# Kernel optimization log

Hardware: AMD Instinct MI355X
Metric: run time of the kernel (lower is better)

The kernel has to match this reference:

```python
import jax, jax.numpy as jnp
import numpy as np

VJ = 80      # vjointnum (groups)
FS = 480     # feature_size = 2*k of RFF
HD = 256     # hidden_dim
K = 240      # RFF k
BATCH = 2048
TWO_PI = 2.0 * np.pi
SLOPE = 0.01  # LeakyReLU default negative_slope


def _wn(v, g):
    # weight_norm (dim=0): w[o,:] = g[o] * v[o,:] / ||v[o,:]||
    return v * (g[:, None] / jnp.linalg.norm(v, axis=1, keepdims=True))


def _grouped(x, v, g, b):
    # x: [B, G, in_g]; v: [G*out_g, in_g]; equivalent to groups=G Conv1d with kernel 1
    w = _wn(v, g)
    out_g = w.shape[0] // VJ
    y = jnp.einsum('bgi,goi->bgo', x, w.reshape(VJ, out_g, -1))
    return y + b.reshape(VJ, out_g)


def _lrelu(t):
    return jnp.where(t >= 0, t, SLOPE * t)


def setup_inputs() -> dict:
    key = jax.random.key(0)
    ks = jax.random.split(key, 12)
    d = {
        'querypoint': jax.random.normal(ks[0], (BATCH, VJ, 3), jnp.float32),
        'point_features': jax.random.normal(ks[1], (BATCH, VJ, FS), jnp.float32),
        'B_rff': jax.random.normal(ks[2], (3, K), jnp.float32),  # std=1
    }
    # per-group layer sizes: 480->512, 512->512, 512->256, 256->6
    dims = [(FS, 2 * HD), (2 * HD, 2 * HD), (2 * HD, HD), (HD, 6)]
    for i, (din, dout) in enumerate(dims):
        d[f'v{i}'] = jax.random.normal(ks[3 + 2 * i], (VJ * dout, din), jnp.float32) * 0.02
        d[f'g{i}'] = jnp.ones((VJ * dout,), jnp.float32)
        d[f'b{i}'] = jnp.zeros((VJ * dout,), jnp.float32)
    return d


def reference(querypoint, point_features, B_rff,
              v0, g0, b0, v1, g1, b1, v2, g2, b2, v3, g3, b3):
    # RFF encode: [B, N, 480]
    emb = TWO_PI * jnp.einsum('bnd,dk->bnk', querypoint, B_rff)
    feat = jnp.concatenate([jnp.cos(emb), jnp.sin(emb)], axis=-1)
    x = point_features + feat                       # [B, 80, 480]
    Bsz = x.shape[0]
    # transpose(-2,-1) then reshape(B, C*N, 1) with groups=80 ==> [B, 80, 480]
    x = jnp.transpose(x, (0, 2, 1)).reshape(Bsz, VJ, FS)
    x = _lrelu(_grouped(x, v0, g0, b0))             # [B, 80, 512]
    x = _lrelu(_grouped(x, v1, g1, b1))             # [B, 80, 512]
    x = _lrelu(_grouped(x, v2, g2, b2))             # [B, 80, 256]
    y = _grouped(x, v3, g3, b3)                     # [B, 80, 6]
    return y.reshape(Bsz, VJ, 6)
```

## Files before the change

### kernel.cpp

```cpp
#include <hip/hip_runtime.h>


typedef __attribute__((ext_vector_type(8))) short short8;
typedef __attribute__((ext_vector_type(4))) float f32x4;
typedef __attribute__((ext_vector_type(4))) unsigned short ushort4v;
typedef __attribute__((ext_vector_type(2))) unsigned int uint2v;

#define VJ    80
#define FS    480
#define HD2   512
#define HD    256
#define BATCH 2048
#define SMLP  528

static __device__ __forceinline__ unsigned short f2bf(float f) {
  unsigned int u = __builtin_bit_cast(unsigned int, f);
  u += 0x7FFFu + ((u >> 16) & 1u);
  return (unsigned short)(u >> 16);
}
static __device__ __forceinline__ float bf2f(unsigned short h) {
  unsigned int u = ((unsigned int)h) << 16;
  return __builtin_bit_cast(float, u);
}

template<int K, int RPG>
static __device__ __forceinline__ void wfrag_body(
    int blk, const float* __restrict__ v, const float* __restrict__ gain,
    unsigned short* __restrict__ dst, float* sV, float* sScale) {
  constexpr int KK = K / 32;
  constexpr int KP = K + 4;
  const int t  = threadIdx.x;
  const int n0 = blk * 16;
  const int g  = n0 / RPG;
  const int ni = (n0 % RPG) >> 4;

  const f32x4* v4 = (const f32x4*)(v + (size_t)n0 * K);
  for (int idx = t; idx < 16 * K / 4; idx += 256) {
    int row = idx / (K / 4), rem = idx - row * (K / 4);
    *(f32x4*)&sV[row * KP + rem * 4] = v4[idx];
  }
  __syncthreads();

  const int wave = t >> 6, lane = t & 63;
  for (int r = wave; r < 16; r += 4) {
    float s = 0.f;
    for (int k = lane; k < K; k += 64) { float x = sV[r * KP + k]; s += x * x; }
    #pragma unroll
    for (int off = 32; off > 0; off >>= 1) s += __shfl_down(s, off);
    if (lane == 0) sScale[r] = gain[n0 + r] / sqrtf(s);
  }
  __syncthreads();

  unsigned short* db = dst + (size_t)g * RPG * K + (size_t)ni * KK * 512;
  for (int o = t; o < 2 * K; o += 256) {
    int f  = o >> 6, l = o & 63;
    int nl = l & 15, k0 = (f << 5) + (((l >> 4) & 3) << 3);
    float sc = sScale[nl];
    short8 pk;
    #pragma unroll
    for (int j = 0; j < 8; ++j) pk[j] = (short)f2bf(sV[nl * KP + k0 + j] * sc);
    *(short8*)&db[(size_t)f * 512 + l * 8] = pk;
  }
}

static __device__ __forceinline__ void wrow_body(
    int blk, const float* __restrict__ v, const float* __restrict__ gain,
    unsigned short* __restrict__ wout, int rows, int din) {
  int row  = blk * 4 + (threadIdx.x >> 6);
  int lane = threadIdx.x & 63;
  if (row >= rows) return;
  const float* vr = v + (size_t)row * din;
  float s = 0.f;
  for (int k = lane; k < din; k += 64) { float x = vr[k]; s += x * x; }
  #pragma unroll
  for (int off = 32; off > 0; off >>= 1) s += __shfl_down(s, off);
  s = __shfl(s, 0);
  float scale = gain[row] / sqrtf(s);
  unsigned short* wr = wout + (size_t)row * din;
  for (int k = lane; k < din; k += 64) wr[k] = f2bf(vr[k] * scale);
}

__global__ void __launch_bounds__(256)
prep_weights(const float* __restrict__ v0, const float* __restrict__ g0,
             const float* __restrict__ v1, const float* __restrict__ g1,
             const float* __restrict__ v2, const float* __restrict__ g2,
             const float* __restrict__ v3, const float* __restrict__ g3,
             unsigned short* __restrict__ W0, unsigned short* __restrict__ W1,
             unsigned short* __restrict__ W2, unsigned short* __restrict__ W3) {
  __shared__ float sV[16 * 516];
  __shared__ float sScale[16];
  const int b = blockIdx.x;
  if      (b < 2560) wfrag_body<480, 512>(b,        v0, g0, W0, sV, sScale);
  else if (b < 5120) wfrag_body<512, 512>(b - 2560, v1, g1, W1, sV, sScale);
  else if (b < 6400) wfrag_body<512, 256>(b - 5120, v2, g2, W2, sV, sScale);
  else               wrow_body(b - 6400, v3, g3, W3, VJ * 6, HD);
}

__global__ void __launch_bounds__(1024)
prep_x(const float* __restrict__ qp, const float* __restrict__ pf,
       const float* __restrict__ Brff, unsigned short* __restrict__ Xg) {
  __shared__ float sB[720];
  __shared__ float sQ[240];
  __shared__ unsigned short sX[480 * 82];
  const int b = blockIdx.x;
  const int t = threadIdx.x;
  if (t < 720) sB[t] = Brff[t];
  if (t < 240) sQ[t] = qp[(size_t)b * 240 + t];
  __syncthreads();
  const float* pfb = pf + (size_t)b * 38400;
  #pragma unroll 2
  for (int idx = t; idx < 19200; idx += 1024) {
    int n2 = idx / 480;
    int c  = idx - n2 * 480;
    int n  = n2 * 2;
    int k  = (c < 240) ? c : c - 240;
    float bx = sB[k], by = sB[240 + k], bz = sB[480 + k];
    float d0 = sQ[n*3]   * bx + sQ[n*3+1] * by + sQ[n*3+2] * bz;
    float d1 = sQ[n*3+3] * bx + sQ[n*3+4] * by + sQ[n*3+5] * bz;
    float f0 = (c < 240) ? __builtin_amdgcn_cosf(d0) : __builtin_amdgcn_sinf(d0);
    float f1 = (c < 240) ? __builtin_amdgcn_cosf(d1) : __builtin_amdgcn_sinf(d1);
    unsigned int w = (unsigned int)f2bf(pfb[n * 480 + c] + f0)
                   | ((unsigned int)f2bf(pfb[(n + 1) * 480 + c] + f1) << 16);
    *(unsigned int*)&sX[c * 82 + n] = w;
  }
  __syncthreads();
  for (int idx4 = t; idx4 < 9600; idx4 += 1024) {
    int g  = idx4 / 120;
    int i4 = idx4 - g * 120;
    int i  = i4 * 4;
    int cl = i / 80;
    int n  = i - cl * 80;
    const unsigned int* p = (const unsigned int*)&sX[(g * 6 + cl) * 82 + n];
    uint2v val = { p[0], p[1] };
    *(uint2v*)(Xg + ((size_t)g * BATCH + b) * 480 + i) = val;
  }
}

#define MLP_STEP(kkv, B)                                                      \
  {                                                                           \
    const int kkc = (kkv);                                                    \
    __builtin_amdgcn_s_setprio(1);                                            \
    _Pragma("unroll")                                                         \
    for (int mi = 0; mi < 4; ++mi) {                                          \
      short8 a = *(const short8*)(aB + mi * 16 * SMLP + kkc * 32);            \
      _Pragma("unroll")                                                       \
      for (int ni = 0; ni < NF; ++ni)                                         \
        acc[mi][ni] = __builtin_amdgcn_mfma_f32_16x16x32_bf16(a, B[ni], acc[mi][ni], 0, 0, 0); \
    }                                                                         \
    __builtin_amdgcn_s_setprio(0);                                            \
    if (kkc + 2 < KK) {                                                       \
      _Pragma("unroll")                                                       \
      for (int ni = 0; ni < NF; ++ni)                                         \
        B[ni] = *(const short8*)(wB + ((size_t)ni * KK + kkc + 2) * 512);     \
    }                                                                         \
  }

template<int K, int N, bool ACT>
static __device__ __forceinline__ void run_layer8(
    unsigned short* __restrict__ s,
    const unsigned short* __restrict__ Wf, const float* __restrict__ bias,
    int wn, int lane) {
  constexpr int NF = N / 128;
  constexpr int KK = K / 32;
  const int nbase = wn * (N / 8);
  const int lr = lane & 15, lh = lane >> 4;

  f32x4 acc[4][NF];
  #pragma unroll
  for (int mi = 0; mi < 4; ++mi)
    #pragma unroll
    for (int ni = 0; ni < NF; ++ni) acc[mi][ni] = (f32x4){0.f, 0.f, 0.f, 0.f};

  const unsigned short* aB = s + lr * SMLP + lh * 8;
  const unsigned short* wB = Wf + (size_t)(wn * NF) * KK * 512 + lane * 8;

  short8 bb0[NF], bb1[NF];
  #pragma unroll
  for (int ni = 0; ni < NF; ++ni) bb0[ni] = *(const short8*)(wB + ((size_t)ni * KK    ) * 512);
  #pragma unroll
  for (int ni = 0; ni < NF; ++ni) bb1[ni] = *(const short8*)(wB + ((size_t)ni * KK + 1) * 512);

  #pragma unroll
  for (int kk2 = 0; kk2 < KK / 2; ++kk2) {
    MLP_STEP(2 * kk2,     bb0);
    MLP_STEP(2 * kk2 + 1, bb1);
  }
  if (KK & 1) MLP_STEP(KK - 1, bb0);

  float bv[NF];
  #pragma unroll
  for (int ni = 0; ni < NF; ++ni) bv[ni] = bias[nbase + ni * 16 + lr];

  __syncthreads();
  #pragma unroll
  for (int mi = 0; mi < 4; ++mi)
    #pragma unroll
    for (int ni = 0; ni < NF; ++ni)
      #pragma unroll
      for (int r = 0; r < 4; ++r) {
        float val = acc[mi][ni][r] + bv[ni];
        if (ACT) val = (val >= 0.f) ? val : 0.01f * val;
        s[(mi * 16 + lh * 4 + r) * SMLP + (nbase + ni * 16 + lr)] = f2bf(val);
      }
  __syncthreads();
}

__global__ void __launch_bounds__(512, 4)
mlp_kernel(const unsigned short* __restrict__ Xg,
           const unsigned short* __restrict__ W0, const unsigned short* __restrict__ W1,
           const unsigned short* __restrict__ W2, const unsigned short* __restrict__ W3,
           const float* __restrict__ b0, const float* __restrict__ b1,
           const float* __restrict__ b2, const float* __restrict__ b3,
           float* __restrict__ out) {
  __shared__ unsigned short s[64 * SMLP];

  const int bid   = blockIdx.x;
  const int xcd   = bid & 7;
  const int local = bid >> 3;
  const int g     = xcd * 10 + (local >> 5);
  const int tile  = local & 31;
  const int m0    = tile * 64;

  const int tid  = threadIdx.x, lane = tid & 63;
  const int wn   = tid >> 6;

  const unsigned short* Xs = Xg + ((size_t)g * BATCH + m0) * 480;
  for (int idx = tid; idx < 64 * 60; idx += 512) {
    int row = idx / 60, c = idx - row * 60;
    *(short8*)&s[row * SMLP + c * 8] = *(const short8*)(Xs + (size_t)row * 480 + c * 8);
  }
  __syncthreads();

  run_layer8<480, 512, true>(s, W0 + (size_t)g * 512 * 480, b0 + g * 512, wn, lane);
  run_layer8<512, 512, true>(s, W1 + (size_t)g * 512 * 512, b1 + g * 512, wn, lane);
  run_layer8<512, 256, true>(s, W2 + (size_t)g * 256 * 512, b2 + g * 256, wn, lane);

  {
    const int m = tid >> 3, o = tid & 7;
    if (o < 6) {
      const unsigned short* hrow = s + m * SMLP;
      const unsigned short* w = W3 + ((size_t)g * 6 + o) * 256;
      float sum = 0.f;
      #pragma unroll 8
      for (int k4 = 0; k4 < 64; ++k4) {
        ushort4v hv = *(const ushort4v*)(hrow + k4 * 4);
        ushort4v wv = *(const ushort4v*)(w + k4 * 4);
        sum += bf2f(hv[0]) * bf2f(wv[0]) + bf2f(hv[1]) * bf2f(wv[1])
             + bf2f(hv[2]) * bf2f(wv[2]) + bf2f(hv[3]) * bf2f(wv[3]);
      }
      out[((size_t)(m0 + m) * VJ + g) * 6 + o] = sum + b3[g * 6 + o];
    }
  }
}

extern "C" void kernel_launch(void* const* d_in, const int* in_sizes, int n_in,
                              void* d_out, int out_size, void* d_ws, size_t ws_size,
                              hipStream_t stream) {
  const float* qp   = (const float*)d_in[0];
  const float* pf   = (const float*)d_in[1];
  const float* Brff = (const float*)d_in[2];
  const float* v0 = (const float*)d_in[3];  const float* g0 = (const float*)d_in[4];  const float* b0 = (const float*)d_in[5];
  const float* v1 = (const float*)d_in[6];  const float* g1 = (const float*)d_in[7];  const float* b1 = (const float*)d_in[8];
  const float* v2 = (const float*)d_in[9];  const float* g2 = (const float*)d_in[10]; const float* b2 = (const float*)d_in[11];
  const float* v3 = (const float*)d_in[12]; const float* g3 = (const float*)d_in[13]; const float* b3 = (const float*)d_in[14];

  unsigned short* W0 = (unsigned short*)d_ws;
  unsigned short* W1 = W0 + (size_t)VJ * HD2 * FS;
  unsigned short* W2 = W1 + (size_t)VJ * HD2 * HD2;
  unsigned short* W3 = W2 + (size_t)VJ * HD  * HD2;
  unsigned short* Xg = W3 + (size_t)VJ * 6 * HD;

  prep_weights<<<dim3(6520), dim3(256), 0, stream>>>(v0, g0, v1, g1, v2, g2, v3, g3,
                                                     W0, W1, W2, W3);
  prep_x<<<dim3(BATCH), dim3(1024), 0, stream>>>(qp, pf, Brff, Xg);
  mlp_kernel<<<dim3(VJ * 32), dim3(512), 0, stream>>>(Xg, W0, W1, W2, W3,
                                                      b0, b1, b2, b3, (float*)d_out);
}
```

Measured before the change: 447.2 us.

## Switch MLP layers to 32x32x16 MFMA tiles and use MFMA for final layer

Rewrites the grouped MLP layers to use 32x32x16 bf16 MFMA instructions with 2 M-tiles per wave, replacing 16x16x32 with 4 M-tiles. The weight prep kernel now emits fragments matching the 32-wide layout with 512-thread blocks. The last 256->6 layer moves from a scalar dot product to a padded 16x16x32 MFMA using a new fragment-packed W3. The aim is fewer LDS A-fragment reads per MFMA and a cheaper final layer, in exchange for larger accumulator register use and more complex output indexing.

```diff
diff --git a/kernel.cpp b/kernel.cpp
--- a/kernel.cpp
+++ b/kernel.cpp
@@ -1,10 +1,11 @@
 #include <hip/hip_runtime.h>
 
 
-typedef __attribute__((ext_vector_type(8))) short short8;
-typedef __attribute__((ext_vector_type(4))) float f32x4;
-typedef __attribute__((ext_vector_type(4))) unsigned short ushort4v;
-typedef __attribute__((ext_vector_type(2))) unsigned int uint2v;
+typedef __attribute__((ext_vector_type(8)))  short short8;
+typedef __attribute__((ext_vector_type(4)))  float f32x4;
+typedef __attribute__((ext_vector_type(16))) float f32x16;
+typedef __attribute__((ext_vector_type(4)))  unsigned short ushort4v;
+typedef __attribute__((ext_vector_type(2)))  unsigned int uint2v;
 
 #define VJ    80
 #define FS    480
@@ -18,31 +19,27 @@
   u += 0x7FFFu + ((u >> 16) & 1u);
   return (unsigned short)(u >> 16);
 }
-static __device__ __forceinline__ float bf2f(unsigned short h) {
-  unsigned int u = ((unsigned int)h) << 16;
-  return __builtin_bit_cast(float, u);
-}
 
 template<int K, int RPG>
-static __device__ __forceinline__ void wfrag_body(
+static __device__ __forceinline__ void wfrag32_body(
     int blk, const float* __restrict__ v, const float* __restrict__ gain,
     unsigned short* __restrict__ dst, float* sV, float* sScale) {
-  constexpr int KK = K / 32;
+  constexpr int KS = K / 16;
   constexpr int KP = K + 4;
   const int t  = threadIdx.x;
-  const int n0 = blk * 16;
+  const int n0 = blk * 32;
   const int g  = n0 / RPG;
-  const int ni = (n0 % RPG) >> 4;
+  const int nt = (n0 % RPG) >> 5;
 
   const f32x4* v4 = (const f32x4*)(v + (size_t)n0 * K);
-  for (int idx = t; idx < 16 * K / 4; idx += 256) {
+  for (int idx = t; idx < 32 * K / 4; idx += 512) {
     int row = idx / (K / 4), rem = idx - row * (K / 4);
     *(f32x4*)&sV[row * KP + rem * 4] = v4[idx];
   }
   __syncthreads();
 
   const int wave = t >> 6, lane = t & 63;
-  for (int r = wave; r < 16; r += 4) {
+  for (int r = wave; r < 32; r += 8) {
     float s = 0.f;
     for (int k = lane; k < K; k += 64) { float x = sV[r * KP + k]; s += x * x; }
     #pragma unroll
@@ -51,49 +48,63 @@
   }
   __syncthreads();
 
-  unsigned short* db = dst + (size_t)g * RPG * K + (size_t)ni * KK * 512;
-  for (int o = t; o < 2 * K; o += 256) {
-    int f  = o >> 6, l = o & 63;
-    int nl = l & 15, k0 = (f << 5) + (((l >> 4) & 3) << 3);
+  unsigned short* db = dst + (size_t)g * RPG * K + (size_t)nt * KS * 512;
+  for (int o = t; o < KS * 64; o += 512) {
+    int ks = o >> 6, l = o & 63;
+    int nl = l & 31, k0 = ks * 16 + ((l >> 5) << 3);
     float sc = sScale[nl];
     short8 pk;
     #pragma unroll
     for (int j = 0; j < 8; ++j) pk[j] = (short)f2bf(sV[nl * KP + k0 + j] * sc);
-    *(short8*)&db[(size_t)f * 512 + l * 8] = pk;
-  }
-}
-
-static __device__ __forceinline__ void wrow_body(
-    int blk, const float* __restrict__ v, const float* __restrict__ gain,
-    unsigned short* __restrict__ wout, int rows, int din) {
-  int row  = blk * 4 + (threadIdx.x >> 6);
-  int lane = threadIdx.x & 63;
-  if (row >= rows) return;
-  const float* vr = v + (size_t)row * din;
-  float s = 0.f;
-  for (int k = lane; k < din; k += 64) { float x = vr[k]; s += x * x; }
-  #pragma unroll
-  for (int off = 32; off > 0; off >>= 1) s += __shfl_down(s, off);
-  s = __shfl(s, 0);
-  float scale = gain[row] / sqrtf(s);
-  unsigned short* wr = wout + (size_t)row * din;
-  for (int k = lane; k < din; k += 64) wr[k] = f2bf(vr[k] * scale);
-}
-
-__global__ void __launch_bounds__(256)
+    *(short8*)&db[(size_t)ks * 512 + l * 8] = pk;
+  }
+}
+
+static __device__ __forceinline__ void w3frag_body(
+    int gidx, const float* __restrict__ v3, const float* __restrict__ g3,
+    unsigned short* __restrict__ W3f, float* sV, float* sScale) {
+  const int t = threadIdx.x;
+  const f32x4* v4 = (const f32x4*)(v3 + (size_t)gidx * 6 * 256);
+  if (t < 384) {
+    int row = t >> 6, rem = t & 63;
+    *(f32x4*)&sV[row * 260 + rem * 4] = v4[t];
+  }
+  __syncthreads();
+  const int wave = t >> 6, lane = t & 63;
+  if (wave < 6) {
+    float s = 0.f;
+    #pragma unroll
+    for (int k = 0; k < 4; ++k) { float x = sV[wave * 260 + lane + k * 64]; s += x * x; }
+    #pragma unroll
+    for (int off = 32; off > 0; off >>= 1) s += __shfl_down(s, off);
+    if (lane == 0) sScale[wave] = g3[gidx * 6 + wave] / sqrtf(s);
+  }
+  __syncthreads();
+  {
+    int ks = t >> 6, l = t & 63;
+    int c = l & 15, k0 = ks * 32 + ((l >> 4) << 3);
+    short8 pk;
+    #pragma unroll
+    for (int j = 0; j < 8; ++j)
+      pk[j] = (c < 6) ? (short)f2bf(sV[c * 260 + k0 + j] * sScale[c]) : (short)0;
+    *(short8*)&W3f[(size_t)gidx * 4096 + (size_t)ks * 512 + l * 8] = pk;
+  }
+}
+
+__global__ void __launch_bounds__(512)
 prep_weights(const float* __restrict__ v0, const float* __restrict__ g0,
              const float* __restrict__ v1, const float* __restrict__ g1,
              const float* __restrict__ v2, const float* __restrict__ g2,
              const float* __restrict__ v3, const float* __restrict__ g3,
              unsigned short* __restrict__ W0, unsigned short* __restrict__ W1,
-             unsigned short* __restrict__ W2, unsigned short* __restrict__ W3) {
-  __shared__ float sV[16 * 516];
-  __shared__ float sScale[16];
+             unsigned short* __restrict__ W2, unsigned short* __restrict__ W3f) {
+  __shared__ float sV[32 * 516];
+  __shared__ float sScale[32];
   const int b = blockIdx.x;
-  if      (b < 2560) wfrag_body<480, 512>(b,        v0, g0, W0, sV, sScale);
-  else if (b < 5120) wfrag_body<512, 512>(b - 2560, v1, g1, W1, sV, sScale);
-  else if (b < 6400) wfrag_body<512, 256>(b - 5120, v2, g2, W2, sV, sScale);
-  else               wrow_body(b - 6400, v3, g3, W3, VJ * 6, HD);
+  if      (b < 1280) wfrag32_body<480, 512>(b,        v0, g0, W0, sV, sScale);
+  else if (b < 2560) wfrag32_body<512, 512>(b - 1280, v1, g1, W1, sV, sScale);
+  else if (b < 3200) wfrag32_body<512, 256>(b - 2560, v2, g2, W2, sV, sScale);
+  else               w3frag_body(b - 3200, v3, g3, W3f, sV, sScale);
 }
 
 __global__ void __launch_bounds__(1024)
@@ -136,71 +147,74 @@
   }
 }
 
-#define MLP_STEP(kkv, B)                                                      \
+#define MLP_STEP32(ksv, BB)                                                   \
   {                                                                           \
-    const int kkc = (kkv);                                                    \
+    const int ksc = (ksv);                                                    \
+    short8 a0 = *(const short8*)(aB + ksc * 16);                              \
+    short8 a1 = *(const short8*)(aB + 32 * SMLP + ksc * 16);                  \
     __builtin_amdgcn_s_setprio(1);                                            \
     _Pragma("unroll")                                                         \
-    for (int mi = 0; mi < 4; ++mi) {                                          \
-      short8 a = *(const short8*)(aB + mi * 16 * SMLP + kkc * 32);            \
+    for (int nt = 0; nt < NT; ++nt)                                           \
+      acc[0][nt] = __builtin_amdgcn_mfma_f32_32x32x16_bf16(a0, BB[nt], acc[0][nt], 0, 0, 0); \
+    _Pragma("unroll")                                                         \
+    for (int nt = 0; nt < NT; ++nt)                                           \
+      acc[1][nt] = __builtin_amdgcn_mfma_f32_32x32x16_bf16(a1, BB[nt], acc[1][nt], 0, 0, 0); \
+    __builtin_amdgcn_s_setprio(0);                                            \
+    if (ksc + 2 < KS) {                                                       \
       _Pragma("unroll")                                                       \
-      for (int ni = 0; ni < NF; ++ni)                                         \
-        acc[mi][ni] = __builtin_amdgcn_mfma_f32_16x16x32_bf16(a, B[ni], acc[mi][ni], 0, 0, 0); \
+      for (int nt = 0; nt < NT; ++nt)                                         \
+        BB[nt] = *(const short8*)(wB + ((size_t)nt * KS + ksc + 2) * 512);    \
     }                                                                         \
-    __builtin_amdgcn_s_setprio(0);                                            \
-    if (kkc + 2 < KK) {                                                       \
-      _Pragma("unroll")                                                       \
-      for (int ni = 0; ni < NF; ++ni)                                         \
-        B[ni] = *(const short8*)(wB + ((size_t)ni * KK + kkc + 2) * 512);     \
-    }                                                                         \
   }
 
 template<int K, int N, bool ACT>
-static __device__ __forceinline__ void run_layer8(
+static __device__ __forceinline__ void run_layer32(
     unsigned short* __restrict__ s,
     const unsigned short* __restrict__ Wf, const float* __restrict__ bias,
     int wn, int lane) {
-  constexpr int NF = N / 128;
-  constexpr int KK = K / 32;
+  constexpr int NT = N / 256;
+  constexpr int KS = K / 16;
   const int nbase = wn * (N / 8);
-  const int lr = lane & 15, lh = lane >> 4;
-
-  f32x4 acc[4][NF];
-  #pragma unroll
-  for (int mi = 0; mi < 4; ++mi)
-    #pragma unroll
-    for (int ni = 0; ni < NF; ++ni) acc[mi][ni] = (f32x4){0.f, 0.f, 0.f, 0.f};
+  const int lr = lane & 31, lh = lane >> 5;
+
+  f32x16 acc[2][NT];
+  #pragma unroll
+  for (int mt = 0; mt < 2; ++mt)
+    #pragma unroll
+    for (int nt = 0; nt < NT; ++nt)
+      #pragma unroll
+      for (int r = 0; r < 16; ++r) acc[mt][nt][r] = 0.f;
 
   const unsigned short* aB = s + lr * SMLP + lh * 8;
-  const unsigned short* wB = Wf + (size_t)(wn * NF) * KK * 512 + lane * 8;
-
-  short8 bb0[NF], bb1[NF];
-  #pragma unroll
-  for (int ni = 0; ni < NF; ++ni) bb0[ni] = *(const short8*)(wB + ((size_t)ni * KK    ) * 512);
-  #pragma unroll
-  for (int ni = 0; ni < NF; ++ni) bb1[ni] = *(const short8*)(wB + ((size_t)ni * KK + 1) * 512);
-
-  #pragma unroll
-  for (int kk2 = 0; kk2 < KK / 2; ++kk2) {
-    MLP_STEP(2 * kk2,     bb0);
-    MLP_STEP(2 * kk2 + 1, bb1);
-  }
-  if (KK & 1) MLP_STEP(KK - 1, bb0);
-
-  float bv[NF];
-  #pragma unroll
-  for (int ni = 0; ni < NF; ++ni) bv[ni] = bias[nbase + ni * 16 + lr];
-
-  __syncthreads();
-  #pragma unroll
-  for (int mi = 0; mi < 4; ++mi)
-    #pragma unroll
-    for (int ni = 0; ni < NF; ++ni)
+  const unsigned short* wB = Wf + (size_t)(wn * NT) * KS * 512 + lane * 8;
+
+  short8 bb0[NT], bb1[NT];
+  #pragma unroll
+  for (int nt = 0; nt < NT; ++nt) bb0[nt] = *(const short8*)(wB + ((size_t)nt * KS    ) * 512);
+  #pragma unroll
+  for (int nt = 0; nt < NT; ++nt) bb1[nt] = *(const short8*)(wB + ((size_t)nt * KS + 1) * 512);
+
+  #pragma unroll
+  for (int ks2 = 0; ks2 < KS / 2; ++ks2) {
+    MLP_STEP32(2 * ks2,     bb0);
+    MLP_STEP32(2 * ks2 + 1, bb1);
+  }
+
+  float bv[NT];
+  #pragma unroll
+  for (int nt = 0; nt < NT; ++nt) bv[nt] = bias[nbase + nt * 32 + lr];
+
+  __syncthreads();
+  #pragma unroll
+  for (int mt = 0; mt < 2; ++mt)
+    #pragma unroll
+    for (int nt = 0; nt < NT; ++nt)
       #pragma unroll
-      for (int r = 0; r < 4; ++r) {
-        float val = acc[mi][ni][r] + bv[ni];
+      for (int r = 0; r < 16; ++r) {
+        float val = acc[mt][nt][r] + bv[nt];
         if (ACT) val = (val >= 0.f) ? val : 0.01f * val;
-        s[(mi * 16 + lh * 4 + r) * SMLP + (nbase + ni * 16 + lr)] = f2bf(val);
+        const int row = mt * 32 + (r & 3) + 8 * (r >> 2) + 4 * lh;
+        s[row * SMLP + (nbase + nt * 32 + lr)] = f2bf(val);
       }
   __syncthreads();
 }
@@ -208,7 +222,7 @@
 __global__ void __launch_bounds__(512, 4)
 mlp_kernel(const unsigned short* __restrict__ Xg,
            const unsigned short* __restrict__ W0, const unsigned short* __restrict__ W1,
-           const unsigned short* __restrict__ W2, const unsigned short* __restrict__ W3,
+           const unsigned short* __restrict__ W2, const unsigned short* __restrict__ W3f,
            const float* __restrict__ b0, const float* __restrict__ b1,
            const float* __restrict__ b2, const float* __restrict__ b3,
            float* __restrict__ out) {
@@ -231,24 +245,27 @@
   }
   __syncthreads();
 
-  run_layer8<480, 512, true>(s, W0 + (size_t)g * 512 * 480, b0 + g * 512, wn, lane);
-  run_layer8<512, 512, true>(s, W1 + (size_t)g * 512 * 512, b1 + g * 512, wn, lane);
-  run_layer8<512, 256, true>(s, W2 + (size_t)g * 256 * 512, b2 + g * 256, wn, lane);
-
-  {
-    const int m = tid >> 3, o = tid & 7;
-    if (o < 6) {
-      const unsigned short* hrow = s + m * SMLP;
-      const unsigned short* w = W3 + ((size_t)g * 6 + o) * 256;
-      float sum = 0.f;
-      #pragma unroll 8
-      for (int k4 = 0; k4 < 64; ++k4) {
-        ushort4v hv = *(const ushort4v*)(hrow + k4 * 4);
-        ushort4v wv = *(const ushort4v*)(w + k4 * 4);
-        sum += bf2f(hv[0]) * bf2f(wv[0]) + bf2f(hv[1]) * bf2f(wv[1])
-             + bf2f(hv[2]) * bf2f(wv[2]) + bf2f(hv[3]) * bf2f(wv[3]);
-      }
-      out[((size_t)(m0 + m) * VJ + g) * 6 + o] = sum + b3[g * 6 + o];
+  run_layer32<480, 512, true>(s, W0 + (size_t)g * 512 * 480, b0 + g * 512, wn, lane);
+  run_layer32<512, 512, true>(s, W1 + (size_t)g * 512 * 512, b1 + g * 512, wn, lane);
+  run_layer32<512, 256, true>(s, W2 + (size_t)g * 256 * 512, b2 + g * 256, wn, lane);
+
+  if (wn < 4) {
+    const int lr = lane & 15, lh = lane >> 4;
+    const unsigned short* aB4 = s + (wn * 16 + lr) * SMLP + lh * 8;
+    const unsigned short* w3  = W3f + (size_t)g * 4096 + lane * 8;
+    f32x4 a4 = (f32x4){0.f, 0.f, 0.f, 0.f};
+    #pragma unroll
+    for (int kk = 0; kk < 8; ++kk) {
+      short8 av  = *(const short8*)(aB4 + kk * 32);
+      short8 wv8 = *(const short8*)(w3 + (size_t)kk * 512);
+      a4 = __builtin_amdgcn_mfma_f32_16x16x32_bf16(av, wv8, a4, 0, 0, 0);
+    }
+    const int col = lane & 15;
+    if (col < 6) {
+      const float bias3 = b3[g * 6 + col];
+      #pragma unroll
+      for (int r = 0; r < 4; ++r)
+        out[((size_t)(m0 + wn * 16 + lh * 4 + r) * VJ + g) * 6 + col] = a4[r] + bias3;
     }
   }
 }
@@ -264,15 +281,15 @@
   const float* v2 = (const float*)d_in[9];  const float* g2 = (const float*)d_in[10]; const float* b2 = (const float*)d_in[11];
   const float* v3 = (const float*)d_in[12]; const float* g3 = (const float*)d_in[13]; const float* b3 = (const float*)d_in[14];
 
-  unsigned short* W0 = (unsigned short*)d_ws;
-  unsigned short* W1 = W0 + (size_t)VJ * HD2 * FS;
-  unsigned short* W2 = W1 + (size_t)VJ * HD2 * HD2;
-  unsigned short* W3 = W2 + (size_t)VJ * HD  * HD2;
-  unsigned short* Xg = W3 + (size_t)VJ * 6 * HD;
-
-  prep_weights<<<dim3(6520), dim3(256), 0, stream>>>(v0, g0, v1, g1, v2, g2, v3, g3,
-                                                     W0, W1, W2, W3);
+  unsigned short* W0  = (unsigned short*)d_ws;
+  unsigned short* W1  = W0 + (size_t)VJ * HD2 * FS;
+  unsigned short* W2  = W1 + (size_t)VJ * HD2 * HD2;
+  unsigned short* W3f = W2 + (size_t)VJ * HD  * HD2;
+  unsigned short* Xg  = W3f + (size_t)VJ * 4096;
+
+  prep_weights<<<dim3(3280), dim3(512), 0, stream>>>(v0, g0, v1, g1, v2, g2, v3, g3,
+                                                     W0, W1, W2, W3f);
   prep_x<<<dim3(BATCH), dim3(1024), 0, stream>>>(qp, pf, Brff, Xg);
-  mlp_kernel<<<dim3(VJ * 32), dim3(512), 0, stream>>>(Xg, W0, W1, W2, W3,
+  mlp_kernel<<<dim3(VJ * 32), dim3(512), 0, stream>>>(Xg, W0, W1, W2, W3f,
                                                       b0, b1, b2, b3, (float*)d_out);
 }
```

New measurement: 415.5 us. 1.08x faster.
